# Kernel tuning notes

Hardware: AMD Instinct MI355X
Metric: run time of the kernel (lower is better)

## Reference

```python
import jax, jax.numpy as jnp
import numpy as np

N_NODES = 10000
N_EDGES = 160000
N_GRAPHS = 64
X_IN = 128
HID = 64
EDGE_DIM = 16
HEADS = 4
# (in_dim, out_dim_per_head) for the 3 TransformerConv layers (concat=False)
DIMS = [(X_IN, HID), (HID, 2 * HID), (2 * HID, HID)]
WNAMES = [f"{n}{l}" for l in (1, 2, 3) for n in ("wq", "bq", "wk", "bk", "wv", "bv", "we", "ws", "bs")]


def setup_inputs() -> dict:
    key = jax.random.key(0)
    ks = iter(jax.random.split(key, 64))
    inp = {}
    inp["x"] = jax.random.normal(next(ks), (N_NODES, X_IN), jnp.float32)
    inp["edge_index"] = jax.random.randint(next(ks), (2, N_EDGES), 0, N_NODES)
    inp["edge_attr"] = jax.random.normal(next(ks), (N_EDGES, EDGE_DIM), jnp.float32)
    inp["batch"] = jnp.sort(jax.random.randint(next(ks), (N_NODES,), 0, N_GRAPHS))
    for l, (din, dout) in enumerate(DIMS, 1):
        hd = HEADS * dout
        for nm, shape in [("wq", (din, hd)), ("wk", (din, hd)), ("wv", (din, hd)),
                          ("we", (EDGE_DIM, hd)), ("ws", (din, dout))]:
            inp[f"{nm}{l}"] = jax.random.normal(next(ks), shape, jnp.float32) * 0.05
        inp[f"bq{l}"] = jnp.zeros((hd,), jnp.float32)
        inp[f"bk{l}"] = jnp.zeros((hd,), jnp.float32)
        inp[f"bv{l}"] = jnp.zeros((hd,), jnp.float32)
        inp[f"bs{l}"] = jnp.zeros((dout,), jnp.float32)
    return inp


def _transformer_conv(x, src, dst, edge_attr, wq, bq, wk, bk, wv, bv, we, ws, bs, dout):
    """PyG TransformerConv, concat=False, root_weight=True, with edge features."""
    N = x.shape[0]
    q = (x @ wq + bq).reshape(N, HEADS, dout)
    k = (x @ wk + bk).reshape(N, HEADS, dout)
    v = (x @ wv + bv).reshape(N, HEADS, dout)
    e = (edge_attr @ we).reshape(-1, HEADS, dout)  # [E, H, C]
    k_j = k[src] + e                               # edge-conditioned keys
    alpha = jnp.einsum("ehd,ehd->eh", q[dst], k_j) * (1.0 / float(dout) ** 0.5)  # [E, H]
    # numerically stable segment softmax over incoming edges of each dst node
    a_max = jax.ops.segment_max(alpha, dst, num_segments=N)
    ex = jnp.exp(alpha - a_max[dst])
    den = jax.ops.segment_sum(ex, dst, num_segments=N)
    attn = ex / den[dst]
    agg = jax.ops.segment_sum((v[src] + e) * attn[..., None], dst, num_segments=N)  # [N, H, C]
    return agg.mean(axis=1) + x @ ws + bs  # concat=False -> head mean; + skip


def _forward(x, edge_attr, edge_index, batch, params):
    src, dst = edge_index[0], edge_index[1]
    h = x
    for l, (_, dout) in enumerate(DIMS, 1):
        p = [params[f"{n}{l}"] for n in ("wq", "bq", "wk", "bk", "wv", "bv", "we", "ws", "bs")]
        h = jax.nn.elu(_transformer_conv(h, src, dst, edge_attr, *p, dout))
    # global mean pool over graphs
    s = jax.ops.segment_sum(h, batch, num_segments=N_GRAPHS)
    cnt = jax.ops.segment_sum(jnp.ones((h.shape[0], 1), h.dtype), batch, num_segments=N_GRAPHS)
    return s / jnp.maximum(cnt, 1.0)


def reference(x, edge_index, edge_attr, batch,
              wq1, bq1, wk1, bk1, wv1, bv1, we1, ws1, bs1,
              wq2, bq2, wk2, bk2, wv2, bv2, we2, ws2, bs2,
              wq3, bq3, wk3, bk3, wv3, bv3, we3, ws3, bs3):
    params = dict(locals())
    return _forward(x, edge_attr, edge_index, batch, params)
```

## Files before the change

kernel.cpp:

```cpp
#include <hip/hip_runtime.h>
#include <hip/hip_fp16.h>
#include <math.h>

#define N_NODES 10000
#define N_EDGES 160000
#define N_GRAPHS 64

using half8 = __attribute__((ext_vector_type(8))) _Float16;
using floatx4 = __attribute__((ext_vector_type(4))) float;

template <int NV> struct KW;
template <> struct KW<1> { using T = uint2; };
template <> struct KW<2> { using T = uint4; };

__device__ inline void cvt_kv(const uint2& w, float4* dst) {
  float2 a = __half22float2(*reinterpret_cast<const __half2*>(&w.x));
  float2 b = __half22float2(*reinterpret_cast<const __half2*>(&w.y));
  dst[0] = make_float4(a.x, a.y, b.x, b.y);
}
__device__ inline void cvt_kv(const uint4& w, float4* dst) {
  float2 a = __half22float2(*reinterpret_cast<const __half2*>(&w.x));
  float2 b = __half22float2(*reinterpret_cast<const __half2*>(&w.y));
  float2 c = __half22float2(*reinterpret_cast<const __half2*>(&w.z));
  float2 d = __half22float2(*reinterpret_cast<const __half2*>(&w.w));
  dst[0] = make_float4(a.x, a.y, b.x, b.y);
  dst[1] = make_float4(c.x, c.y, d.x, d.y);
}

__device__ inline void load_kv_pair(const __half* rb, uint2& kr, uint2& vr) {
  uint4 w = *reinterpret_cast<const uint4*>(rb);
  kr = make_uint2(w.x, w.y);
  vr = make_uint2(w.z, w.w);
}
__device__ inline void load_kv_pair(const __half* rb, uint4& kr, uint4& vr) {
  kr = *reinterpret_cast<const uint4*>(rb);
  vr = *reinterpret_cast<const uint4*>(rb + 8);
}

template <int K, int HD, int DOUT>
__global__ __launch_bounds__(256) void gemm_mfma(
    const __half* __restrict__ A, const __half* __restrict__ Wp,
    const float* __restrict__ bias, __half* __restrict__ QS,
    __half* __restrict__ KV, int M) {
  constexpr int QSS = HD + 64 + DOUT;
  constexpr int KVS = 2 * HD;
  constexpr int NV = DOUT / 64;
  constexpr int KS = K / 32;
  __shared__ __half st[64][72];
  const int tid = threadIdx.x;
  const int wave = tid >> 6, lane = tid & 63;
  const int quad = lane >> 4, n16 = lane & 15;
  const int row0 = blockIdx.y * 64;
  const int col0 = blockIdx.x * 64;
  const int nblk0 = blockIdx.x * 4;

  const int arow = min(row0 + wave * 16 + n16, M - 1);
  half8 afrag[KS];
#pragma unroll
  for (int s = 0; s < KS; ++s)
    afrag[s] = *reinterpret_cast<const half8*>(A + (size_t)arow * K + s * 32 + quad * 8);

  floatx4 acc[4];
#pragma unroll
  for (int t = 0; t < 4; ++t) {
    acc[t] = (floatx4){0.f, 0.f, 0.f, 0.f};
#pragma unroll
    for (int s = 0; s < KS; ++s) {
      half8 bf = *reinterpret_cast<const half8*>(
          Wp + (((size_t)(nblk0 + t) * KS + s) * 64 + lane) * 8);
      acc[t] = __builtin_amdgcn_mfma_f32_16x16x32_f16(afrag[s], bf, acc[t], 0, 0, 0);
    }
  }

#pragma unroll
  for (int t = 0; t < 4; ++t) {
    float bv = bias[col0 + t * 16 + n16];
#pragma unroll
    for (int r = 0; r < 4; ++r)
      st[wave * 16 + quad * 4 + r][t * 16 + n16] = __float2half(acc[t][r] + bv);
  }
  __syncthreads();

  if (col0 < HD + 64 || col0 >= 3 * HD + 64) {
    const int qcol = (col0 < HD + 64) ? col0 : (HD + 64 + (col0 - 3 * HD - 64));
    for (int c = tid; c < 512; c += 256) {
      int r = c >> 3, seg = c & 7;
      int row = row0 + r;
      if (row < M)
        *reinterpret_cast<uint4*>(QS + (size_t)row * QSS + qcol + seg * 8) =
            *reinterpret_cast<const uint4*>(&st[r][seg * 8]);
    }
  } else {
    constexpr int G = 4 * NV;
    constexpr int NG = 64 / G;
    const int ckv0 = col0 - (HD + 64);
    for (int c = tid; c < 64 * NG; c += 256) {
      int r = c / NG, gl = c % NG;
      int row = row0 + r;
      if (row >= M) continue;
      int ckv = ckv0 + gl * G;
      int off;
      if (ckv < HD) off = (ckv / G) * (2 * G);
      else          off = ((ckv - HD) / G) * (2 * G) + G;
      if (NV == 1)
        *reinterpret_cast<uint2*>(KV + (size_t)row * KVS + off) =
            *reinterpret_cast<const uint2*>(&st[r][gl * G]);
      else
        *reinterpret_cast<uint4*>(KV + (size_t)row * KVS + off) =
            *reinterpret_cast<const uint4*>(&st[r][gl * G]);
    }
  }
}

__device__ inline void pack_layer(int i, int K, int HD, int DOUT, float scale,
                                  const float* wq, const float* wk,
                                  const float* wv, const float* wsk,
                                  const float* we, const float* bq,
                                  const float* bk, const float* bv,
                                  const float* bs, __half* Wp, float* bcat) {
  const int W = 3 * HD + DOUT + 64;
  const int KS = K / 32;
  if (i < K * W) {
    int j = i & 7, lane = (i >> 3) & 63, fs = i >> 9;
    int nblk = fs / KS, s = fs - nblk * KS;
    int quad = lane >> 4, n = lane & 15;
    int k = s * 32 + quad * 8 + j, c = nblk * 16 + n;
    float v;
    if (c < HD) {
      v = wq[k * HD + c] * scale;
    } else if (c < HD + 64) {
      int gi = c - HD, hh = gi >> 4, d = gi & 15;
      float a = 0.f;
      for (int cc = 0; cc < DOUT; ++cc)
        a += wq[k * HD + hh * DOUT + cc] * we[d * HD + hh * DOUT + cc];
      v = a * scale;
    } else if (c < 2 * HD + 64) {
      v = wk[k * HD + (c - HD - 64)];
    } else if (c < 3 * HD + 64) {
      v = wv[k * HD + (c - 2 * HD - 64)];
    } else {
      v = wsk[k * DOUT + (c - 3 * HD - 64)];
    }
    Wp[i] = __float2half(v);
  } else {
    int c = i - K * W;
    float v;
    if (c < HD) {
      v = bq[c] * scale;
    } else if (c < HD + 64) {
      int gi = c - HD, hh = gi >> 4, d = gi & 15;
      float a = 0.f;
      for (int cc = 0; cc < DOUT; ++cc)
        a += bq[hh * DOUT + cc] * we[d * HD + hh * DOUT + cc];
      v = a * scale;
    } else if (c < 2 * HD + 64) {
      v = bk[c - HD - 64];
    } else if (c < 3 * HD + 64) {
      v = bv[c - 2 * HD - 64];
    } else {
      v = bs[c - 3 * HD - 64];
    }
    bcat[c] = v;
  }
}

#define T1 115584
#define T2 227904
#define T3 343488
#define TCONV (N_NODES * 32)
#define TTOT (T3 + TCONV)

__global__ void pack_all(
    const float* wq1, const float* wk1, const float* wv1, const float* ws1,
    const float* we1, const float* bq1, const float* bk1, const float* bv1,
    const float* bs1,
    const float* wq2, const float* wk2, const float* wv2, const float* ws2,
    const float* we2, const float* bq2, const float* bk2, const float* bv2,
    const float* bs2,
    const float* wq3, const float* wk3, const float* wv3, const float* ws3,
    const float* we3, const float* bq3, const float* bk3, const float* bv3,
    const float* bs3,
    __half* W1, float* b1, __half* W2, float* b2, __half* W3, float* b3,
    const float* x, __half* x16) {
  const float SC1 = 0.125f, SC2 = 0.08838834764831845f;
  for (int i = blockIdx.x * blockDim.x + threadIdx.x; i < TTOT;
       i += gridDim.x * blockDim.x) {
    if (i < T1)
      pack_layer(i, 128, 256, 64, SC1, wq1, wk1, wv1, ws1, we1, bq1, bk1, bv1, bs1, W1, b1);
    else if (i < T2)
      pack_layer(i - T1, 64, 512, 128, SC2, wq2, wk2, wv2, ws2, we2, bq2, bk2, bv2, bs2, W2, b2);
    else if (i < T3)
      pack_layer(i - T2, 128, 256, 64, SC1, wq3, wk3, wv3, ws3, we3, bq3, bk3, bv3, bs3, W3, b3);
    else {
      int k = i - T3;
      float4 v = reinterpret_cast<const float4*>(x)[k];
      __half2* o = reinterpret_cast<__half2*>(x16) + 2 * k;
      o[0] = __floats2half2_rn(v.x, v.y);
      o[1] = __floats2half2_rn(v.z, v.w);
    }
  }
}

__global__ void count_dst(const int* __restrict__ dst, int* __restrict__ cnt) {
  int e = blockIdx.x * blockDim.x + threadIdx.x;
  if (e < N_EDGES) atomicAdd(&cnt[dst[e]], 1);
}

__global__ __launch_bounds__(1024) void scan_offs(const int* __restrict__ cnt,
                                                  int* __restrict__ offs) {
  __shared__ int part[1024];
  const int t = threadIdx.x;
  const int chunk = (N_NODES + 1023) / 1024;
  const int b = t * chunk;
  const int e = min(N_NODES, b + chunk);
  int s = 0;
  for (int i = b; i < e; ++i) s += cnt[i];
  part[t] = s;
  __syncthreads();
  for (int off = 1; off < 1024; off <<= 1) {
    int v = (t >= off) ? part[t - off] : 0;
    __syncthreads();
    part[t] += v;
    __syncthreads();
  }
  int pre = (t == 0) ? 0 : part[t - 1];
  for (int i = b; i < e; ++i) { offs[i] = pre; pre += cnt[i]; }
  if (t == 0) offs[N_NODES] = part[1023];
}

__global__ void scatter_csr(const int* __restrict__ src, const int* __restrict__ dst,
                            const float* __restrict__ edge_attr,
                            const int* __restrict__ offs, int* __restrict__ cursor,
                            int* __restrict__ csr_src, float* __restrict__ csr_ea) {
  int e = blockIdx.x * blockDim.x + threadIdx.x;
  if (e < N_EDGES) {
    int d = dst[e];
    int pos = offs[d] + atomicAdd(&cursor[d], 1);
    csr_src[pos] = src[e];
    float4* o4 = reinterpret_cast<float4*>(csr_ea + (size_t)pos * 16);
    const float4* s4 = reinterpret_cast<const float4*>(edge_attr + (size_t)e * 16);
    o4[0] = s4[0]; o4[1] = s4[1]; o4[2] = s4[2]; o4[3] = s4[3];
  }
}

template <int DOUT>
__global__ __launch_bounds__(256) void edge_attn(
    const __half* __restrict__ QS, const __half* __restrict__ KV,
    const float* __restrict__ we, const int* __restrict__ csr_src,
    const float* __restrict__ csr_ea, const int* __restrict__ offs,
    float* __restrict__ out, __half* __restrict__ out16) {
  constexpr int HD = 4 * DOUT;
  constexpr int QSS = HD + 64 + DOUT;
  constexpr int KVS = 2 * HD;
  constexpr int NV = DOUT / 64;
  using KWT = typename KW<NV>::T;

  __shared__ float sacc[2][HD];
  __shared__ float sl[2][64], stc[2][64];

  const int lane = threadIdx.x & 63;
  const int wid = threadIdx.x >> 6;
  const int nl = wid >> 1, half = wid & 1;
  const int h = lane >> 4, t16 = lane & 15;
  const int n = blockIdx.x * 2 + nl;
  const int c0 = t16 * 4 * NV;
  const int bofs = (h * 16 + t16) * 8 * NV;

  const __half* base = QS + (size_t)n * QSS;
  float4 q[NV], acc[NV];
  {
    KWT qw = *reinterpret_cast<const KWT*>(base + h * DOUT + c0);
    cvt_kv(qw, q);
  }
#pragma unroll
  for (int v = 0; v < NV; ++v) acc[v] = make_float4(0.f, 0.f, 0.f, 0.f);
  const float g = __half2float(base[HD + h * 16 + t16]);

  float lsum = 0.f, tacc = 0.f;

  const int s0 = offs[n], s1 = offs[n + 1];
  const int end_full = s0 + ((s1 - s0) & ~3);

  int sjA[4], sjB[4];
  float eaA[4], eaB[4];
  KWT krA[4], vrA[4], krB[4], vrB[4];

  auto load_grp = [&](int bi, int (&sj)[4], float (&ea)[4], KWT (&kr)[4],
                      KWT (&vr)[4]) {
#pragma unroll
    for (int j = 0; j < 4; ++j) sj[j] = csr_src[bi + j];
#pragma unroll
    for (int j = 0; j < 4; ++j) ea[j] = csr_ea[(size_t)(bi + j) * 16 + t16];
#pragma unroll
    for (int j = 0; j < 4; ++j)
      load_kv_pair(KV + (size_t)sj[j] * KVS + bofs, kr[j], vr[j]);
  };

  auto compute_grp = [&](float (&ea)[4], KWT (&kr)[4], KWT (&vr)[4]) {
    float a[4];
#pragma unroll
    for (int j = 0; j < 4; ++j) {
      float4 kk[NV];
      cvt_kv(kr[j], kk);
      float p = ea[j] * g;
#pragma unroll
      for (int v = 0; v < NV; ++v)
        p += q[v].x * kk[v].x + q[v].y * kk[v].y + q[v].z * kk[v].z +
             q[v].w * kk[v].w;
      a[j] = p;
    }
#pragma unroll
    for (int j = 0; j < 4; ++j) {
      a[j] += __shfl_xor(a[j], 1);
      a[j] += __shfl_xor(a[j], 2);
      a[j] += __shfl_xor(a[j], 4);
      a[j] += __shfl_xor(a[j], 8);
    }
    float p0 = __expf(a[0]), p1 = __expf(a[1]);
    float p2 = __expf(a[2]), p3 = __expf(a[3]);
    lsum += p0 + p1 + p2 + p3;
    tacc += p0 * ea[0] + p1 * ea[1] + p2 * ea[2] + p3 * ea[3];
    float pj[4] = {p0, p1, p2, p3};
#pragma unroll
    for (int j = 0; j < 4; ++j) {
      float4 vv[NV];
      cvt_kv(vr[j], vv);
#pragma unroll
      for (int v = 0; v < NV; ++v) {
        acc[v].x += pj[j] * vv[v].x;
        acc[v].y += pj[j] * vv[v].y;
        acc[v].z += pj[j] * vv[v].z;
        acc[v].w += pj[j] * vv[v].w;
      }
    }
  };

  int ii = s0 + half * 4;
  if (ii < end_full) {
    load_grp(ii, sjA, eaA, krA, vrA);
    for (;;) {
      int nx = ii + 8;
      if (nx >= end_full) { compute_grp(eaA, krA, vrA); break; }
      load_grp(nx, sjB, eaB, krB, vrB);
      compute_grp(eaA, krA, vrA);
      ii = nx; nx = ii + 8;
      if (nx >= end_full) { compute_grp(eaB, krB, vrB); break; }
      load_grp(nx, sjA, eaA, krA, vrA);
      compute_grp(eaB, krB, vrB);
      ii = nx;
    }
  }

  if (half == 0) {
    for (int t = end_full; t < s1; ++t) {
      int s = csr_src[t];
      float ea0 = csr_ea[(size_t)t * 16 + t16];
      KWT kw, vw;
      load_kv_pair(KV + (size_t)s * KVS + bofs, kw, vw);
      float4 kk[NV], vv[NV];
      cvt_kv(kw, kk);
      cvt_kv(vw, vv);
      float a = ea0 * g;
#pragma unroll
      for (int v = 0; v < NV; ++v)
        a += q[v].x * kk[v].x + q[v].y * kk[v].y + q[v].z * kk[v].z + q[v].w * kk[v].w;
      a += __shfl_xor(a, 1);
      a += __shfl_xor(a, 2);
      a += __shfl_xor(a, 4);
      a += __shfl_xor(a, 8);
      float p = __expf(a);
      lsum += p;
      tacc += p * ea0;
#pragma unroll
      for (int v = 0; v < NV; ++v) {
        acc[v].x += p * vv[v].x;
        acc[v].y += p * vv[v].y;
        acc[v].z += p * vv[v].z;
        acc[v].w += p * vv[v].w;
      }
    }
  }

  if (half == 1) {
#pragma unroll
    for (int v = 0; v < NV; ++v) {
      int cb = h * DOUT + c0 + 4 * v;
      sacc[nl][cb + 0] = acc[v].x;
      sacc[nl][cb + 1] = acc[v].y;
      sacc[nl][cb + 2] = acc[v].z;
      sacc[nl][cb + 3] = acc[v].w;
    }
    sl[nl][lane] = lsum;
    stc[nl][lane] = tacc;
  }
  __syncthreads();
  if (half != 0) return;

  lsum += sl[nl][lane];
  tacc += stc[nl][lane];
#pragma unroll
  for (int v = 0; v < NV; ++v) {
    int cb = h * DOUT + c0 + 4 * v;
    acc[v].x += sacc[nl][cb + 0];
    acc[v].y += sacc[nl][cb + 1];
    acc[v].z += sacc[nl][cb + 2];
    acc[v].w += sacc[nl][cb + 3];
  }

  float invl = (lsum > 0.f) ? 1.f / lsum : 0.f;
  float tn = tacc * invl;
  float4 val[NV];
#pragma unroll
  for (int v = 0; v < NV; ++v) {
    val[v].x = acc[v].x * invl; val[v].y = acc[v].y * invl;
    val[v].z = acc[v].z * invl; val[v].w = acc[v].w * invl;
  }
#pragma unroll
  for (int d = 0; d < 16; ++d) {
    float td = __shfl(tn, (lane & 48) | d);
    const float* wb = we + d * HD + h * DOUT + c0;
#pragma unroll
    for (int v = 0; v < NV; ++v) {
      float4 w4 = *reinterpret_cast<const float4*>(wb + 4 * v);
      val[v].x += td * w4.x; val[v].y += td * w4.y;
      val[v].z += td * w4.z; val[v].w += td * w4.w;
    }
  }
#pragma unroll
  for (int v = 0; v < NV; ++v) {
    val[v].x += __shfl_xor(val[v].x, 16); val[v].x += __shfl_xor(val[v].x, 32);
    val[v].y += __shfl_xor(val[v].y, 16); val[v].y += __shfl_xor(val[v].y, 32);
    val[v].z += __shfl_xor(val[v].z, 16); val[v].z += __shfl_xor(val[v].z, 32);
    val[v].w += __shfl_xor(val[v].w, 16); val[v].w += __shfl_xor(val[v].w, 32);
  }
  if (h == 0) {
    KWT sw = *reinterpret_cast<const KWT*>(base + HD + 64 + c0);
    float4 sk[NV];
    cvt_kv(sw, sk);
#pragma unroll
    for (int v = 0; v < NV; ++v) {
      float4 o;
      o.x = 0.25f * val[v].x + sk[v].x;
      o.y = 0.25f * val[v].y + sk[v].y;
      o.z = 0.25f * val[v].z + sk[v].z;
      o.w = 0.25f * val[v].w + sk[v].w;
      o.x = (o.x > 0.f) ? o.x : expm1f(o.x);
      o.y = (o.y > 0.f) ? o.y : expm1f(o.y);
      o.z = (o.z > 0.f) ? o.z : expm1f(o.z);
      o.w = (o.w > 0.f) ? o.w : expm1f(o.w);
      *reinterpret_cast<float4*>(out + (size_t)n * DOUT + c0 + 4 * v) = o;
      __half2* o16 = reinterpret_cast<__half2*>(out16 + (size_t)n * DOUT + c0 + 4 * v);
      o16[0] = __floats2half2_rn(o.x, o.y);
      o16[1] = __floats2half2_rn(o.z, o.w);
    }
  }
}

__device__ inline int lower_bound(const int* b, int n, int v) {
  int lo = 0, hi = n;
  while (lo < hi) {
    int mid = (lo + hi) >> 1;
    if (b[mid] < v) lo = mid + 1; else hi = mid;
  }
  return lo;
}

__global__ __launch_bounds__(256) void pool_all(const float* __restrict__ h,
                                                const int* __restrict__ batch,
                                                float* __restrict__ out) {
  const int g = blockIdx.x;
  const int start = lower_bound(batch, N_NODES, g);
  const int end = lower_bound(batch, N_NODES, g + 1);
  const int c = threadIdx.x & 63, j = threadIdx.x >> 6;
  float s = 0.f;
  for (int n = start + j; n < end; n += 4) s += h[(size_t)n * 64 + c];
  __shared__ float red[4][64];
  red[j][c] = s;
  __syncthreads();
  if (j == 0) {
    float tot = red[0][c] + red[1][c] + red[2][c] + red[3][c];
    out[g * 64 + c] = tot / (float)max(end - start, 1);
  }
}

extern "C" void kernel_launch(void* const* d_in, const int* in_sizes, int n_in,
                              void* d_out, int out_size, void* d_ws, size_t ws_size,
                              hipStream_t stream) {
  const float* x = (const float*)d_in[0];
  const int* edge_index = (const int*)d_in[1];
  const float* edge_attr = (const float*)d_in[2];
  const int* batch = (const int*)d_in[3];
  const int* srcp = edge_index;
  const int* dstp = edge_index + N_EDGES;

  const bool dict_order = in_sizes[5] > 1024;
  const float *wq[3], *wk[3], *wv[3], *wep[3], *wsk[3], *bq[3], *bk[3], *bv[3], *bs[3];
  for (int L = 0; L < 3; ++L) {
    int b = 4 + L * 9;
    if (dict_order) {
      wq[L] = (const float*)d_in[b + 0];
      wk[L] = (const float*)d_in[b + 1];
      wv[L] = (const float*)d_in[b + 2];
      wep[L] = (const float*)d_in[b + 3];
      wsk[L] = (const float*)d_in[b + 4];
      bq[L] = (const float*)d_in[b + 5];
      bk[L] = (const float*)d_in[b + 6];
      bv[L] = (const float*)d_in[b + 7];
      bs[L] = (const float*)d_in[b + 8];
    } else {
      wq[L] = (const float*)d_in[b + 0];
      bq[L] = (const float*)d_in[b + 1];
      wk[L] = (const float*)d_in[b + 2];
      bk[L] = (const float*)d_in[b + 3];
      wv[L] = (const float*)d_in[b + 4];
      bv[L] = (const float*)d_in[b + 5];
      wep[L] = (const float*)d_in[b + 6];
      wsk[L] = (const float*)d_in[b + 7];
      bs[L] = (const float*)d_in[b + 8];
    }
  }

  char* p = (char*)d_ws;
  __half* qs = (__half*)p;    p += (size_t)N_NODES * 704 * 2;
  __half* kv = (__half*)p;    p += (size_t)N_NODES * 1024 * 2;
  float* h1 = (float*)p;      p += (size_t)N_NODES * 64 * 4;
  float* h2 = (float*)p;      p += (size_t)N_NODES * 128 * 4;
  __half* x16 = (__half*)p;   p += (size_t)N_NODES * 128 * 2;
  __half* h16 = (__half*)p;   p += (size_t)N_NODES * 128 * 2;
  __half* W1 = (__half*)p;    p += 128 * 896 * 2;
  __half* W2 = (__half*)p;    p += 64 * 1728 * 2;
  __half* W3 = (__half*)p;    p += 128 * 896 * 2;
  float* b1 = (float*)p;      p += 896 * 4;
  float* b2 = (float*)p;      p += 1728 * 4;
  float* b3 = (float*)p;      p += 896 * 4;
  float* csr_ea = (float*)p;  p += (size_t)N_EDGES * 16 * 4;
  int* cnt = (int*)p;         p += N_NODES * 4;
  int* cursor = (int*)p;      p += N_NODES * 4;
  int* offs = (int*)p;        p += (N_NODES + 1) * 4;
  int* csr_src = (int*)p;     p += N_EDGES * 4;

  pack_all<<<1024, 256, 0, stream>>>(
      wq[0], wk[0], wv[0], wsk[0], wep[0], bq[0], bk[0], bv[0], bs[0],
      wq[1], wk[1], wv[1], wsk[1], wep[1], bq[1], bk[1], bv[1], bs[1],
      wq[2], wk[2], wv[2], wsk[2], wep[2], bq[2], bk[2], bv[2], bs[2],
      W1, b1, W2, b2, W3, b3, x, x16);

  hipMemsetAsync(cnt, 0, 2 * N_NODES * sizeof(int), stream);
  count_dst<<<(N_EDGES + 255) / 256, 256, 0, stream>>>(dstp, cnt);
  scan_offs<<<1, 1024, 0, stream>>>(cnt, offs);
  scatter_csr<<<(N_EDGES + 255) / 256, 256, 0, stream>>>(srcp, dstp, edge_attr,
                                                         offs, cursor, csr_src, csr_ea);

  const int MT = (N_NODES + 63) / 64;
  gemm_mfma<128, 256, 64><<<dim3(896 / 64, MT), 256, 0, stream>>>(x16, W1, b1, qs,
                                                                  kv, N_NODES);
  edge_attn<64><<<N_NODES / 2, 256, 0, stream>>>(qs, kv, wep[0], csr_src, csr_ea,
                                                 offs, h1, h16);
  gemm_mfma<64, 512, 128><<<dim3(1728 / 64, MT), 256, 0, stream>>>(h16, W2, b2, qs,
                                                                   kv, N_NODES);
  edge_attn<128><<<N_NODES / 2, 256, 0, stream>>>(qs, kv, wep[1], csr_src, csr_ea,
                                                  offs, h2, h16);
  gemm_mfma<128, 256, 64><<<dim3(896 / 64, MT), 256, 0, stream>>>(h16, W3, b3, qs,
                                                                  kv, N_NODES);
  edge_attn<64><<<N_NODES / 2, 256, 0, stream>>>(qs, kv, wep[2], csr_src, csr_ea,
                                                 offs, h1, x16 );

  pool_all<<<N_GRAPHS, 256, 0, stream>>>(h1, batch, (float*)d_out);
}
```

Baseline: 374.3 us.

## Use one wave per node in edge attention with wave-shared edge index loads

Edge attention now gives each destination node a single wavefront instead of splitting its edges across two waves. That removes the shared-memory reduction and the block barrier, and each block handles four nodes instead of two. Source indices are loaded once per 64-edge chunk and broadcast with shuffles, and edge attributes are loaded coalesced across the wave and then shuffled. For DOUT=64 the group size grows to 8 edges to keep more gathers in flight. The tradeoff is less parallelism per high-degree node, more register pressure and more shuffle traffic.

Measured after the change: 364.3 us. -2.7%, faster.

```diff
diff --git a/kernel.cpp b/kernel.cpp
--- a/kernel.cpp
+++ b/kernel.cpp
@@ -25,16 +25,6 @@
   float2 d = __half22float2(*reinterpret_cast<const __half2*>(&w.w));
   dst[0] = make_float4(a.x, a.y, b.x, b.y);
   dst[1] = make_float4(c.x, c.y, d.x, d.y);
-}
-
-__device__ inline void load_kv_pair(const __half* rb, uint2& kr, uint2& vr) {
-  uint4 w = *reinterpret_cast<const uint4*>(rb);
-  kr = make_uint2(w.x, w.y);
-  vr = make_uint2(w.z, w.w);
-}
-__device__ inline void load_kv_pair(const __half* rb, uint4& kr, uint4& vr) {
-  kr = *reinterpret_cast<const uint4*>(rb);
-  vr = *reinterpret_cast<const uint4*>(rb + 8);
 }
 
 template <int K, int HD, int DOUT>
@@ -253,16 +243,14 @@
   constexpr int QSS = HD + 64 + DOUT;
   constexpr int KVS = 2 * HD;
   constexpr int NV = DOUT / 64;
+  constexpr int EPG = (NV == 1) ? 8 : 4;
+  constexpr int NEA = EPG / 4;
+  constexpr int NVR = (NV == 2) ? EPG : 1;
   using KWT = typename KW<NV>::T;
 
-  __shared__ float sacc[2][HD];
-  __shared__ float sl[2][64], stc[2][64];
-
   const int lane = threadIdx.x & 63;
-  const int wid = threadIdx.x >> 6;
-  const int nl = wid >> 1, half = wid & 1;
   const int h = lane >> 4, t16 = lane & 15;
-  const int n = blockIdx.x * 2 + nl;
+  const int n = blockIdx.x * 4 + (threadIdx.x >> 6);
   const int c0 = t16 * 4 * NV;
   const int bofs = (h * 16 + t16) * 8 * NV;
 
@@ -279,30 +267,41 @@
   float lsum = 0.f, tacc = 0.f;
 
   const int s0 = offs[n], s1 = offs[n + 1];
-  const int end_full = s0 + ((s1 - s0) & ~3);
-
-  int sjA[4], sjB[4];
-  float eaA[4], eaB[4];
-  KWT krA[4], vrA[4], krB[4], vrB[4];
-
-  auto load_grp = [&](int bi, int (&sj)[4], float (&ea)[4], KWT (&kr)[4],
-                      KWT (&vr)[4]) {
-#pragma unroll
-    for (int j = 0; j < 4; ++j) sj[j] = csr_src[bi + j];
-#pragma unroll
-    for (int j = 0; j < 4; ++j) ea[j] = csr_ea[(size_t)(bi + j) * 16 + t16];
-#pragma unroll
-    for (int j = 0; j < 4; ++j)
-      load_kv_pair(KV + (size_t)sj[j] * KVS + bofs, kr[j], vr[j]);
+  const int deg = s1 - s0;
+  const int gend = s0 + (deg & ~(EPG - 1));
+
+  int srcv = 0;
+  float eavA[NEA], eavB[NEA];
+  uint4 krA[EPG], krB[EPG];
+  uint4 vrA[NVR], vrB[NVR];
+
+  auto load_grp = [&](int bi, int rel, float (&eav)[NEA], uint4 (&kr)[EPG],
+                      uint4 (&vr)[NVR]) {
+#pragma unroll
+    for (int u = 0; u < NEA; ++u)
+      eav[u] = csr_ea[(size_t)(bi + 4 * u) * 16 + lane];
+#pragma unroll
+    for (int j = 0; j < EPG; ++j) {
+      int sj = __shfl(srcv, rel + j);
+      const __half* rb = KV + (size_t)sj * KVS + bofs;
+      kr[j] = *reinterpret_cast<const uint4*>(rb);
+      if (NV == 2) vr[j % NVR] = *reinterpret_cast<const uint4*>(rb + 8);
+    }
   };
 
-  auto compute_grp = [&](float (&ea)[4], KWT (&kr)[4], KWT (&vr)[4]) {
-    float a[4];
-#pragma unroll
-    for (int j = 0; j < 4; ++j) {
+  auto compute_grp = [&](float (&eav)[NEA], uint4 (&kr)[EPG], uint4 (&vr)[NVR]) {
+    float a[EPG], eat[EPG];
+#pragma unroll
+    for (int j = 0; j < EPG; ++j) {
+      eat[j] = __shfl(eav[j >> 2], ((j & 3) << 4) | t16);
       float4 kk[NV];
-      cvt_kv(kr[j], kk);
-      float p = ea[j] * g;
+      if (NV == 1) {
+        uint2 kw = make_uint2(kr[j].x, kr[j].y);
+        cvt_kv(kw, kk);
+      } else {
+        cvt_kv(kr[j], kk);
+      }
+      float p = eat[j] * g;
 #pragma unroll
       for (int v = 0; v < NV; ++v)
         p += q[v].x * kk[v].x + q[v].y * kk[v].y + q[v].z * kk[v].z +
@@ -310,101 +309,88 @@
       a[j] = p;
     }
 #pragma unroll
-    for (int j = 0; j < 4; ++j) {
+    for (int j = 0; j < EPG; ++j) {
       a[j] += __shfl_xor(a[j], 1);
       a[j] += __shfl_xor(a[j], 2);
       a[j] += __shfl_xor(a[j], 4);
       a[j] += __shfl_xor(a[j], 8);
     }
-    float p0 = __expf(a[0]), p1 = __expf(a[1]);
-    float p2 = __expf(a[2]), p3 = __expf(a[3]);
-    lsum += p0 + p1 + p2 + p3;
-    tacc += p0 * ea[0] + p1 * ea[1] + p2 * ea[2] + p3 * ea[3];
-    float pj[4] = {p0, p1, p2, p3};
-#pragma unroll
-    for (int j = 0; j < 4; ++j) {
+    float p[EPG];
+#pragma unroll
+    for (int j = 0; j < EPG; ++j) {
+      p[j] = __expf(a[j]);
+      lsum += p[j];
+      tacc += p[j] * eat[j];
+    }
+#pragma unroll
+    for (int j = 0; j < EPG; ++j) {
       float4 vv[NV];
-      cvt_kv(vr[j], vv);
+      if (NV == 1) {
+        uint2 vw = make_uint2(kr[j].z, kr[j].w);
+        cvt_kv(vw, vv);
+      } else {
+        cvt_kv(vr[j % NVR], vv);
+      }
 #pragma unroll
       for (int v = 0; v < NV; ++v) {
-        acc[v].x += pj[j] * vv[v].x;
-        acc[v].y += pj[j] * vv[v].y;
-        acc[v].z += pj[j] * vv[v].z;
-        acc[v].w += pj[j] * vv[v].w;
+        acc[v].x += p[j] * vv[v].x;
+        acc[v].y += p[j] * vv[v].y;
+        acc[v].z += p[j] * vv[v].z;
+        acc[v].w += p[j] * vv[v].w;
       }
     }
   };
 
-  int ii = s0 + half * 4;
-  if (ii < end_full) {
-    load_grp(ii, sjA, eaA, krA, vrA);
+  for (int cbase = s0; cbase < gend; cbase += 64) {
+    const int cend = min(cbase + 64, gend);
+    srcv = csr_src[min(cbase + lane, s1 - 1)];
+    int ii = cbase;
+    load_grp(ii, 0, eavA, krA, vrA);
     for (;;) {
-      int nx = ii + 8;
-      if (nx >= end_full) { compute_grp(eaA, krA, vrA); break; }
-      load_grp(nx, sjB, eaB, krB, vrB);
-      compute_grp(eaA, krA, vrA);
-      ii = nx; nx = ii + 8;
-      if (nx >= end_full) { compute_grp(eaB, krB, vrB); break; }
-      load_grp(nx, sjA, eaA, krA, vrA);
-      compute_grp(eaB, krB, vrB);
+      int nx = ii + EPG;
+      if (nx >= cend) { compute_grp(eavA, krA, vrA); break; }
+      load_grp(nx, nx - cbase, eavB, krB, vrB);
+      compute_grp(eavA, krA, vrA);
+      ii = nx; nx = ii + EPG;
+      if (nx >= cend) { compute_grp(eavB, krB, vrB); break; }
+      load_grp(nx, nx - cbase, eavA, krA, vrA);
+      compute_grp(eavB, krB, vrB);
       ii = nx;
     }
   }
 
-  if (half == 0) {
-    for (int t = end_full; t < s1; ++t) {
-      int s = csr_src[t];
-      float ea0 = csr_ea[(size_t)t * 16 + t16];
-      KWT kw, vw;
-      load_kv_pair(KV + (size_t)s * KVS + bofs, kw, vw);
-      float4 kk[NV], vv[NV];
+  for (int t = gend; t < s1; ++t) {
+    int s = csr_src[t];
+    float ea0 = csr_ea[(size_t)t * 16 + t16];
+    const __half* rb = KV + (size_t)s * KVS + bofs;
+    float4 kk[NV], vv[NV];
+    if (NV == 1) {
+      uint4 w = *reinterpret_cast<const uint4*>(rb);
+      uint2 kw = make_uint2(w.x, w.y), vw = make_uint2(w.z, w.w);
       cvt_kv(kw, kk);
       cvt_kv(vw, vv);
-      float a = ea0 * g;
-#pragma unroll
-      for (int v = 0; v < NV; ++v)
-        a += q[v].x * kk[v].x + q[v].y * kk[v].y + q[v].z * kk[v].z + q[v].w * kk[v].w;
-      a += __shfl_xor(a, 1);
-      a += __shfl_xor(a, 2);
-      a += __shfl_xor(a, 4);
-      a += __shfl_xor(a, 8);
-      float p = __expf(a);
-      lsum += p;
-      tacc += p * ea0;
-#pragma unroll
-      for (int v = 0; v < NV; ++v) {
-        acc[v].x += p * vv[v].x;
-        acc[v].y += p * vv[v].y;
-        acc[v].z += p * vv[v].z;
-        acc[v].w += p * vv[v].w;
-      }
-    }
-  }
-
-  if (half == 1) {
+    } else {
+      cvt_kv(*reinterpret_cast<const uint4*>(rb), kk);
+      cvt_kv(*reinterpret_cast<const uint4*>(rb + 8), vv);
+    }
+    float a = ea0 * g;
+#pragma unroll
+    for (int v = 0; v < NV; ++v)
+      a += q[v].x * kk[v].x + q[v].y * kk[v].y + q[v].z * kk[v].z + q[v].w * kk[v].w;
+    a += __shfl_xor(a, 1);
+    a += __shfl_xor(a, 2);
+    a += __shfl_xor(a, 4);
+    a += __shfl_xor(a, 8);
+    float p = __expf(a);
+    lsum += p;
+    tacc += p * ea0;
 #pragma unroll
     for (int v = 0; v < NV; ++v) {
-      int cb = h * DOUT + c0 + 4 * v;
-      sacc[nl][cb + 0] = acc[v].x;
-      sacc[nl][cb + 1] = acc[v].y;
-      sacc[nl][cb + 2] = acc[v].z;
-      sacc[nl][cb + 3] = acc[v].w;
-    }
-    sl[nl][lane] = lsum;
-    stc[nl][lane] = tacc;
-  }
-  __syncthreads();
-  if (half != 0) return;
-
-  lsum += sl[nl][lane];
-  tacc += stc[nl][lane];
-#pragma unroll
-  for (int v = 0; v < NV; ++v) {
-    int cb = h * DOUT + c0 + 4 * v;
-    acc[v].x += sacc[nl][cb + 0];
-    acc[v].y += sacc[nl][cb + 1];
-    acc[v].z += sacc[nl][cb + 2];
-    acc[v].w += sacc[nl][cb + 3];
+      acc[v].x += p * vv[v].x;
+      acc[v].y += p * vv[v].y;
+      acc[v].z += p * vv[v].z;
+      acc[v].w += p * vv[v].w;
+    }
   }
 
   float invl = (lsum > 0.f) ? 1.f / lsum : 0.f;
@@ -537,7 +523,7 @@
   int* cnt = (int*)p;         p += N_NODES * 4;
   int* cursor = (int*)p;      p += N_NODES * 4;
   int* offs = (int*)p;        p += (N_NODES + 1) * 4;
-  int* csr_src = (int*)p;     p += N_EDGES * 4;
+  int* csr_src = (int*)p;     p += (N_EDGES + 64) * 4;
 
   pack_all<<<1024, 256, 0, stream>>>(
       wq[0], wk[0], wv[0], wsk[0], wep[0], bq[0], bk[0], bv[0], bs[0],
@@ -554,15 +540,15 @@
   const int MT = (N_NODES + 63) / 64;
   gemm_mfma<128, 256, 64><<<dim3(896 / 64, MT), 256, 0, stream>>>(x16, W1, b1, qs,
                                                                   kv, N_NODES);
-  edge_attn<64><<<N_NODES / 2, 256, 0, stream>>>(qs, kv, wep[0], csr_src, csr_ea,
+  edge_attn<64><<<N_NODES / 4, 256, 0, stream>>>(qs, kv, wep[0], csr_src, csr_ea,
                                                  offs, h1, h16);
   gemm_mfma<64, 512, 128><<<dim3(1728 / 64, MT), 256, 0, stream>>>(h16, W2, b2, qs,
                                                                    kv, N_NODES);
-  edge_attn<128><<<N_NODES / 2, 256, 0, stream>>>(qs, kv, wep[1], csr_src, csr_ea,
+  edge_attn<128><<<N_NODES / 4, 256, 0, stream>>>(qs, kv, wep[1], csr_src, csr_ea,
                                                   offs, h2, h16);
   gemm_mfma<128, 256, 64><<<dim3(896 / 64, MT), 256, 0, stream>>>(h16, W3, b3, qs,
                                                                   kv, N_NODES);
-  edge_attn<64><<<N_NODES / 2, 256, 0, stream>>>(qs, kv, wep[2], csr_src, csr_ea,
+  edge_attn<64><<<N_NODES / 4, 256, 0, stream>>>(qs, kv, wep[2], csr_src, csr_ea,
                                                  offs, h1, x16 );
 
   pool_all<<<N_GRAPHS, 256, 0, stream>>>(h1, batch, (float*)d_out);
```
